# Kernel optimization log

Measured on AMD Instinct MI355X. Metric: run time of the kernel, lower is better.

## Reference

```python
import jax, jax.numpy as jnp
import numpy as np

B, S, W = 2, 2048, 1024
HEADS = 16
ATTN_CH = W // HEADS  # 64
SCALE = 1.0 / np.sqrt(np.sqrt(ATTN_CH))


def setup_inputs() -> dict:
    key = jax.random.key(0)
    ks = jax.random.split(key, 5)
    init_scale = 0.25
    x = jax.random.normal(ks[0], (B, S, W), dtype=jnp.float32)
    w_qkv = jax.random.normal(ks[1], (3 * W, W), dtype=jnp.float32) * init_scale
    b_qkv = jnp.zeros((3 * W,), dtype=jnp.float32)
    w_proj = jax.random.normal(ks[2], (W, W), dtype=jnp.float32) * init_scale
    b_proj = jnp.zeros((W,), dtype=jnp.float32)
    return {"x": x, "w_qkv": w_qkv, "b_qkv": b_qkv, "w_proj": w_proj, "b_proj": b_proj}


def reference(x, w_qkv, b_qkv, w_proj, b_proj):
    bs, n_ctx, width = x.shape
    # c_qkv: Linear(width -> 3*width)
    qkv = jnp.einsum('bsw,ow->bso', x, w_qkv) + b_qkv  # [b, s, 3*width]
    # view as [b, s, heads, 3*attn_ch] then split
    qkv = qkv.reshape(bs, n_ctx, HEADS, 3 * ATTN_CH)
    q, k, v = jnp.split(qkv, 3, axis=-1)  # each [b, s, h, c]
    # symmetric scaling by 1/attn_ch**0.25 on q and k
    weight = jnp.einsum('bthc,bshc->bhts', q * SCALE, k * SCALE)
    weight = jax.nn.softmax(weight.astype(jnp.float32), axis=-1).astype(q.dtype)
    out = jnp.einsum('bhts,bshc->bthc', weight, v).reshape(bs, n_ctx, -1)
    # c_proj: Linear(width -> width)
    return jnp.einsum('bsw,ow->bso', out, w_proj) + b_proj
```

## Files before the change

### kernel.cpp

```cpp
#include <hip/hip_runtime.h>

typedef unsigned short U16;
typedef __attribute__((ext_vector_type(8))) short bf16x8;
typedef __attribute__((ext_vector_type(4))) float f32x4;
typedef __attribute__((ext_vector_type(4))) unsigned short u16x4;

#define BB 2
#define SS 2048
#define WW 1024
#define HH 16
#define CC 64
#define MTOT (BB*SS)
#define SCALE 0.35355339059327373f
#define LOG2E 1.4426950408889634f

__device__ __forceinline__ U16 f2bf(float f) {
  unsigned int u = __float_as_uint(f);
  u = (u + 0x7fffu + ((u >> 16) & 1u)) >> 16;
  return (U16)u;
}
__device__ __forceinline__ float bf2f(U16 h) {
  return __uint_as_float(((unsigned int)h) << 16);
}

#define GLD16(gp, lp) __builtin_amdgcn_global_load_lds( \
    (const __attribute__((address_space(1))) unsigned int*)(gp), \
    (__attribute__((address_space(3))) unsigned int*)(lp), 16, 0, 0)

#define MFMA(a,b,c) __builtin_amdgcn_mfma_f32_16x16x32_bf16(a,b,c,0,0,0)

__global__ void cvt_split(const float* __restrict__ in, U16* __restrict__ hi,
                          U16* __restrict__ lo, int n4) {
  int i = blockIdx.x * blockDim.x + threadIdx.x;
  if (i < n4) {
    float4 v = reinterpret_cast<const float4*>(in)[i];
    float vv[4] = {v.x, v.y, v.z, v.w};
    u16x4 h, l;
#pragma unroll
    for (int j = 0; j < 4; ++j) {
      U16 hb = f2bf(vv[j]);
      h[j] = hb;
      l[j] = f2bf(vv[j] - bf2f(hb));
    }
    reinterpret_cast<u16x4*>(hi)[i] = h;
    reinterpret_cast<u16x4*>(lo)[i] = l;
  }
}

template<int EPI>
__global__ __launch_bounds__(256) void gemm_split(
    const U16* __restrict__ Ah, const U16* __restrict__ Al,
    const U16* __restrict__ Bh, const U16* __restrict__ Bl,
    const float* __restrict__ bias, int K, int N,
    float* __restrict__ out,
    U16* __restrict__ Qh, U16* __restrict__ Ql,
    U16* __restrict__ Kh, U16* __restrict__ Kl, U16* __restrict__ Vt)
{
  __shared__ U16 AsH[128*32], AsL[128*32], BsH[128*32], BsL[128*32];
  const int tid  = threadIdx.x;
  const int lane = tid & 63, w = tid >> 6;
  const int wr = w >> 1, wc = w & 1;
  const int g = lane >> 4, lr = lane & 15;
  const int bm = blockIdx.x, bn = blockIdx.y;

  f32x4 acc[4][4] = {};

  for (int k0 = 0; k0 < K; k0 += 32) {
#pragma unroll
    for (int i = 0; i < 2; ++i) {
      const int rowT = i*64 + (tid >> 2);
      const int sblk = (tid & 3) ^ ((rowT >> 1) & 3);
      const size_t ga = (size_t)(bm*128 + rowT) * K + k0 + sblk*8;
      const size_t gb = (size_t)(bn*128 + rowT) * K + k0 + sblk*8;
      const int lb = i*2048 + w*512;
      GLD16(Ah + ga, &AsH[lb]);
      GLD16(Al + ga, &AsL[lb]);
      GLD16(Bh + gb, &BsH[lb]);
      GLD16(Bl + gb, &BsL[lb]);
    }
    __syncthreads();

    bf16x8 ah[4], al[4], bh[4], bl[4];
#pragma unroll
    for (int mi = 0; mi < 4; ++mi) {
      const int row = wr*64 + mi*16 + lr;
      const int so  = row*32 + ((g ^ ((row >> 1) & 3)) * 8);
      ah[mi] = *reinterpret_cast<const bf16x8*>(&AsH[so]);
      al[mi] = *reinterpret_cast<const bf16x8*>(&AsL[so]);
    }
#pragma unroll
    for (int ni = 0; ni < 4; ++ni) {
      const int row = wc*64 + ni*16 + lr;
      const int so  = row*32 + ((g ^ ((row >> 1) & 3)) * 8);
      bh[ni] = *reinterpret_cast<const bf16x8*>(&BsH[so]);
      bl[ni] = *reinterpret_cast<const bf16x8*>(&BsL[so]);
    }
#pragma unroll
    for (int ni = 0; ni < 4; ++ni)
#pragma unroll
      for (int mi = 0; mi < 4; ++mi) {
        acc[mi][ni] = MFMA(ah[mi], bh[ni], acc[mi][ni]);
        acc[mi][ni] = MFMA(ah[mi], bl[ni], acc[mi][ni]);
        acc[mi][ni] = MFMA(al[mi], bh[ni], acc[mi][ni]);
      }
    __syncthreads();
  }

#pragma unroll
  for (int mi = 0; mi < 4; ++mi) {
#pragma unroll
    for (int ni = 0; ni < 4; ++ni) {
#pragma unroll
      for (int r = 0; r < 4; ++r) {
        const int grow = bm*128 + wr*64 + mi*16 + 4*g + r;
        const int gcol = bn*128 + wc*64 + ni*16 + lr;
        const float val = acc[mi][ni][r] + bias[gcol];
        if (EPI == 0) {
          const int b = grow >> 11, s = grow & 2047;
          const int h = gcol / 192;
          const int rem = gcol - h * 192;
          const int t = rem >> 6, c = rem & 63;
          const size_t bh_ = (size_t)(b * HH + h);
          if (t == 2) {
            Vt[(bh_ * CC + c) * SS + s] = f2bf(val);
          } else {
            const float sv = val * SCALE;
            const U16 hb = f2bf(sv);
            const U16 lb = f2bf(sv - bf2f(hb));
            const size_t idx = (bh_ * SS + s) * CC + c;
            if (t == 0) { Qh[idx] = hb; Ql[idx] = lb; }
            else        { Kh[idx] = hb; Kl[idx] = lb; }
          }
        } else {
          out[(size_t)grow * N + gcol] = val;
        }
      }
    }
  }
}

__global__ __launch_bounds__(256) void attn_kernel(
    const U16* __restrict__ Qh, const U16* __restrict__ Ql,
    const U16* __restrict__ Kh, const U16* __restrict__ Kl,
    const U16* __restrict__ Vtb, U16* __restrict__ Obh, U16* __restrict__ Obl)
{
  __shared__ U16 KsH[64*64];
  __shared__ U16 KsL[64*64];
  __shared__ U16 Vts[64*64];
  __shared__ U16 Ps [4][16*72];

  const int tid  = threadIdx.x;
  const int lane = tid & 63, w = tid >> 6;
  const int g = lane >> 4, lr = lane & 15;
  const int bh = blockIdx.x;
  const int qt = blockIdx.y;

  const U16* QhP = Qh  + (size_t)bh * SS * CC;
  const U16* QlP = Ql  + (size_t)bh * SS * CC;
  const U16* KhP = Kh  + (size_t)bh * SS * CC;
  const U16* KlP = Kl  + (size_t)bh * SS * CC;
  const U16* Vh  = Vtb + (size_t)bh * CC * SS;

  const int q0 = qt * 64 + w * 16;

  bf16x8 qfh[2], qfl[2];
#pragma unroll
  for (int kk = 0; kk < 2; ++kk) {
    qfh[kk] = *reinterpret_cast<const bf16x8*>(&QhP[(size_t)(q0 + lr) * CC + kk*32 + g*8]);
    qfl[kk] = *reinterpret_cast<const bf16x8*>(&QlP[(size_t)(q0 + lr) * CC + kk*32 + g*8]);
  }

  float m[4], l[4];
  f32x4 o[4];
#pragma unroll
  for (int r = 0; r < 4; ++r) { m[r] = -1e30f; l[r] = 0.f; }
#pragma unroll
  for (int cs = 0; cs < 4; ++cs) o[cs] = (f32x4){0.f, 0.f, 0.f, 0.f};

  for (int kv = 0; kv < SS; kv += 64) {
#pragma unroll
    for (int i = 0; i < 2; ++i) {
      const int t2   = i*256 + tid;
      const int row  = t2 >> 3;
      const int sblk = (t2 & 7) ^ (row & 7);
      const int lb   = (i*256 + w*64) * 8;
      GLD16(KhP + (size_t)(kv + row) * CC + sblk*8, &KsH[lb]);
      GLD16(KlP + (size_t)(kv + row) * CC + sblk*8, &KsL[lb]);
      GLD16(Vh  + (size_t)row * SS + kv + sblk*8,   &Vts[lb]);
    }
    __syncthreads();

    f32x4 sacc[4];
#pragma unroll
    for (int ns = 0; ns < 4; ++ns) {
      f32x4 a = {0.f, 0.f, 0.f, 0.f};
      const int krow = ns*16 + lr;
#pragma unroll
      for (int kk = 0; kk < 2; ++kk) {
        const int so = krow*64 + (((kk*4 + g) ^ (krow & 7)) * 8);
        bf16x8 kfh = *reinterpret_cast<const bf16x8*>(&KsH[so]);
        bf16x8 kfl = *reinterpret_cast<const bf16x8*>(&KsL[so]);
        a = MFMA(qfh[kk], kfh, a);
        a = MFMA(qfh[kk], kfl, a);
        a = MFMA(qfl[kk], kfh, a);
      }
      sacc[ns] = a;
    }

    float pr[4][4];
#pragma unroll
    for (int r = 0; r < 4; ++r) {
      float mx = fmaxf(fmaxf(sacc[0][r], sacc[1][r]), fmaxf(sacc[2][r], sacc[3][r]));
#pragma unroll
      for (int off = 1; off < 16; off <<= 1) mx = fmaxf(mx, __shfl_xor(mx, off, 64));
      const float mn   = fmaxf(m[r], mx);
      const float corr = exp2f((m[r] - mn) * LOG2E);
      float ps = 0.f;
#pragma unroll
      for (int ns = 0; ns < 4; ++ns) {
        const float p = exp2f((sacc[ns][r] - mn) * LOG2E);
        pr[ns][r] = p; ps += p;
      }
#pragma unroll
      for (int off = 1; off < 16; off <<= 1) ps += __shfl_xor(ps, off, 64);
      l[r] = l[r] * corr + ps;
      m[r] = mn;
#pragma unroll
      for (int cs = 0; cs < 4; ++cs) o[cs][r] *= corr;
    }

#pragma unroll
    for (int ns = 0; ns < 4; ++ns)
#pragma unroll
      for (int r = 0; r < 4; ++r)
        Ps[w][(4*g + r)*72 + ns*16 + lr] = f2bf(pr[ns][r]);
    asm volatile("s_waitcnt lgkmcnt(0)" ::: "memory");
    __builtin_amdgcn_sched_barrier(0);

    bf16x8 pf[2];
#pragma unroll
    for (int kk = 0; kk < 2; ++kk)
      pf[kk] = *reinterpret_cast<const bf16x8*>(&Ps[w][lr*72 + kk*32 + g*8]);
#pragma unroll
    for (int cs = 0; cs < 4; ++cs) {
      f32x4 a = o[cs];
      const int vrow = cs*16 + lr;
#pragma unroll
      for (int kk = 0; kk < 2; ++kk) {
        const int so = vrow*64 + (((kk*4 + g) ^ (vrow & 7)) * 8);
        bf16x8 vf = *reinterpret_cast<const bf16x8*>(&Vts[so]);
        a = MFMA(pf[kk], vf, a);
      }
      o[cs] = a;
    }
    __syncthreads();
  }

  const int b = bh >> 4, h = bh & 15;
#pragma unroll
  for (int r = 0; r < 4; ++r) {
    const float inv = 1.0f / l[r];
    const int qg = q0 + 4*g + r;
#pragma unroll
    for (int cs = 0; cs < 4; ++cs) {
      const float ov = o[cs][r] * inv;
      const size_t idx = ((size_t)(b*SS + qg)) * WW + h*CC + cs*16 + lr;
      const U16 hb = f2bf(ov);
      Obh[idx] = hb;
      Obl[idx] = f2bf(ov - bf2f(hb));
    }
  }
}

extern "C" void kernel_launch(void* const* d_in, const int* in_sizes, int n_in,
                              void* d_out, int out_size, void* d_ws, size_t ws_size,
                              hipStream_t stream)
{
  const float* x      = (const float*)d_in[0];
  const float* w_qkv  = (const float*)d_in[1];
  const float* b_qkv  = (const float*)d_in[2];
  const float* w_proj = (const float*)d_in[3];
  const float* b_proj = (const float*)d_in[4];
  float* out = (float*)d_out;

  U16* ws = (U16*)d_ws;
  U16* xh      = ws;
  U16* xl      = xh     + (size_t)MTOT*WW;
  U16* wqkvh   = xl     + (size_t)MTOT*WW;
  U16* wqkvl   = wqkvh  + (size_t)3*WW*WW;
  U16* wprojh  = wqkvl  + (size_t)3*WW*WW;
  U16* wprojl  = wprojh + (size_t)WW*WW;
  U16* Qhb     = wprojl + (size_t)WW*WW;
  U16* Qlb     = Qhb    + (size_t)BB*HH*SS*CC;
  U16* Khb     = Qlb    + (size_t)BB*HH*SS*CC;
  U16* Klb     = Khb    + (size_t)BB*HH*SS*CC;
  U16* Vtb     = Klb    + (size_t)BB*HH*SS*CC;
  U16* Obh     = xh;
  U16* Obl     = xl;

  int n4 = MTOT*WW/4;
  cvt_split<<<(n4 + 255)/256, 256, 0, stream>>>(x, xh, xl, n4);
  n4 = 3*WW*WW/4;
  cvt_split<<<(n4 + 255)/256, 256, 0, stream>>>(w_qkv, wqkvh, wqkvl, n4);
  n4 = WW*WW/4;
  cvt_split<<<(n4 + 255)/256, 256, 0, stream>>>(w_proj, wprojh, wprojl, n4);

  gemm_split<0><<<dim3(MTOT/128, (3*WW)/128), 256, 0, stream>>>(
      xh, xl, wqkvh, wqkvl, b_qkv, WW, 3*WW, nullptr,
      Qhb, Qlb, Khb, Klb, Vtb);

  attn_kernel<<<dim3(BB*HH, SS/64), 256, 0, stream>>>(
      Qhb, Qlb, Khb, Klb, Vtb, Obh, Obl);

  gemm_split<1><<<dim3(MTOT/128, WW/128), 256, 0, stream>>>(
      Obh, Obl, wprojh, wprojl, b_proj, WW, WW, out,
      nullptr, nullptr, nullptr, nullptr, nullptr);
}
```

Baseline: 378.2 us.

## Load low-part operands directly from global and add lazy softmax rescaling

```diff
diff --git a/kernel.cpp b/kernel.cpp
--- a/kernel.cpp
+++ b/kernel.cpp
@@ -1,4 +1,5 @@
 #include <hip/hip_runtime.h>
+#include <hip/hip_bf16.h>
 
 typedef unsigned short U16;
 typedef __attribute__((ext_vector_type(8))) short bf16x8;
@@ -11,13 +12,12 @@
 #define HH 16
 #define CC 64
 #define MTOT (BB*SS)
-#define SCALE 0.35355339059327373f
-#define LOG2E 1.4426950408889634f
+#define QK_SCALE 0.4246609001440095f
+#define RESCALE_THR 8.0f
 
 __device__ __forceinline__ U16 f2bf(float f) {
-  unsigned int u = __float_as_uint(f);
-  u = (u + 0x7fffu + ((u >> 16) & 1u)) >> 16;
-  return (U16)u;
+  __hip_bfloat16 b = __float2bfloat16(f);
+  return *reinterpret_cast<U16*>(&b);
 }
 __device__ __forceinline__ float bf2f(U16 h) {
   return __uint_as_float(((unsigned int)h) << 16);
@@ -56,7 +56,7 @@
     U16* __restrict__ Qh, U16* __restrict__ Ql,
     U16* __restrict__ Kh, U16* __restrict__ Kl, U16* __restrict__ Vt)
 {
-  __shared__ U16 AsH[128*32], AsL[128*32], BsH[128*32], BsL[128*32];
+  __shared__ U16 AsH[128*32], BsH[128*32];
   const int tid  = threadIdx.x;
   const int lane = tid & 63, w = tid >> 6;
   const int wr = w >> 1, wc = w & 1;
@@ -74,32 +74,32 @@
       const size_t gb = (size_t)(bn*128 + rowT) * K + k0 + sblk*8;
       const int lb = i*2048 + w*512;
       GLD16(Ah + ga, &AsH[lb]);
-      GLD16(Al + ga, &AsL[lb]);
       GLD16(Bh + gb, &BsH[lb]);
-      GLD16(Bl + gb, &BsL[lb]);
     }
     __syncthreads();
 
-    bf16x8 ah[4], al[4], bh[4], bl[4];
+    bf16x8 ah[4], bh[4], al[4], bl[4];
 #pragma unroll
     for (int mi = 0; mi < 4; ++mi) {
       const int row = wr*64 + mi*16 + lr;
-      const int so  = row*32 + ((g ^ ((row >> 1) & 3)) * 8);
-      ah[mi] = *reinterpret_cast<const bf16x8*>(&AsH[so]);
-      al[mi] = *reinterpret_cast<const bf16x8*>(&AsL[so]);
+      ah[mi] = *reinterpret_cast<const bf16x8*>(&AsH[row*32 + ((g ^ ((row >> 1) & 3)) * 8)]);
+      al[mi] = *reinterpret_cast<const bf16x8*>(Al + (size_t)(bm*128 + row) * K + k0 + g*8);
     }
 #pragma unroll
     for (int ni = 0; ni < 4; ++ni) {
       const int row = wc*64 + ni*16 + lr;
-      const int so  = row*32 + ((g ^ ((row >> 1) & 3)) * 8);
-      bh[ni] = *reinterpret_cast<const bf16x8*>(&BsH[so]);
-      bl[ni] = *reinterpret_cast<const bf16x8*>(&BsL[so]);
+      bh[ni] = *reinterpret_cast<const bf16x8*>(&BsH[row*32 + ((g ^ ((row >> 1) & 3)) * 8)]);
+      bl[ni] = *reinterpret_cast<const bf16x8*>(Bl + (size_t)(bn*128 + row) * K + k0 + g*8);
     }
 #pragma unroll
     for (int ni = 0; ni < 4; ++ni)
 #pragma unroll
+      for (int mi = 0; mi < 4; ++mi)
+        acc[mi][ni] = MFMA(ah[mi], bh[ni], acc[mi][ni]);
+#pragma unroll
+    for (int ni = 0; ni < 4; ++ni)
+#pragma unroll
       for (int mi = 0; mi < 4; ++mi) {
-        acc[mi][ni] = MFMA(ah[mi], bh[ni], acc[mi][ni]);
         acc[mi][ni] = MFMA(ah[mi], bl[ni], acc[mi][ni]);
         acc[mi][ni] = MFMA(al[mi], bh[ni], acc[mi][ni]);
       }
@@ -124,7 +124,7 @@
           if (t == 2) {
             Vt[(bh_ * CC + c) * SS + s] = f2bf(val);
           } else {
-            const float sv = val * SCALE;
+            const float sv = val * QK_SCALE;
             const U16 hb = f2bf(sv);
             const U16 lb = f2bf(sv - bf2f(hb));
             const size_t idx = (bh_ * SS + s) * CC + c;
@@ -207,26 +207,48 @@
       sacc[ns] = a;
     }
 
+    float mx[4];
+#pragma unroll
+    for (int r = 0; r < 4; ++r) {
+      float v = fmaxf(fmaxf(sacc[0][r], sacc[1][r]), fmaxf(sacc[2][r], sacc[3][r]));
+#pragma unroll
+      for (int off = 1; off < 16; off <<= 1) v = fmaxf(v, __shfl_xor(v, off, 64));
+      mx[r] = v;
+    }
     float pr[4][4];
-#pragma unroll
-    for (int r = 0; r < 4; ++r) {
-      float mx = fmaxf(fmaxf(sacc[0][r], sacc[1][r]), fmaxf(sacc[2][r], sacc[3][r]));
-#pragma unroll
-      for (int off = 1; off < 16; off <<= 1) mx = fmaxf(mx, __shfl_xor(mx, off, 64));
-      const float mn   = fmaxf(m[r], mx);
-      const float corr = exp2f((m[r] - mn) * LOG2E);
-      float ps = 0.f;
-#pragma unroll
-      for (int ns = 0; ns < 4; ++ns) {
-        const float p = exp2f((sacc[ns][r] - mn) * LOG2E);
-        pr[ns][r] = p; ps += p;
-      }
-#pragma unroll
-      for (int off = 1; off < 16; off <<= 1) ps += __shfl_xor(ps, off, 64);
-      l[r] = l[r] * corr + ps;
-      m[r] = mn;
-#pragma unroll
-      for (int cs = 0; cs < 4; ++cs) o[cs][r] *= corr;
+    const bool nog = (mx[0] <= m[0] + RESCALE_THR) & (mx[1] <= m[1] + RESCALE_THR) &
+                     (mx[2] <= m[2] + RESCALE_THR) & (mx[3] <= m[3] + RESCALE_THR);
+    if (__all(nog)) {
+#pragma unroll
+      for (int r = 0; r < 4; ++r) {
+        float ps = 0.f;
+#pragma unroll
+        for (int ns = 0; ns < 4; ++ns) {
+          const float p = exp2f(sacc[ns][r] - m[r]);
+          pr[ns][r] = p; ps += p;
+        }
+#pragma unroll
+        for (int off = 1; off < 16; off <<= 1) ps += __shfl_xor(ps, off, 64);
+        l[r] += ps;
+      }
+    } else {
+#pragma unroll
+      for (int r = 0; r < 4; ++r) {
+        const float mn   = fmaxf(m[r], mx[r]);
+        const float corr = exp2f(m[r] - mn);
+        float ps = 0.f;
+#pragma unroll
+        for (int ns = 0; ns < 4; ++ns) {
+          const float p = exp2f(sacc[ns][r] - mn);
+          pr[ns][r] = p; ps += p;
+        }
+#pragma unroll
+        for (int off = 1; off < 16; off <<= 1) ps += __shfl_xor(ps, off, 64);
+        l[r] = l[r] * corr + ps;
+        m[r] = mn;
+#pragma unroll
+        for (int cs = 0; cs < 4; ++cs) o[cs][r] *= corr;
+      }
     }
 
 #pragma unroll
```

Measured after the change: 418.6 us. 10.7% more time.
